# Performance work log

Measured on AMD Instinct MI355X. Metric: run time of the kernel, lower is better.

## Reference

```python
import jax, jax.numpy as jnp
import numpy as np

D = 64       # feature_dim
C = 64       # number of classes
NS = 1024    # support samples (16 shots per class)
NQ = 32768   # query samples
REG = 0.3    # reg_param
KAPPA0 = 1.0 / 600.0  # gamma_m from _num_images=600


def _l2norm(x):
    # torch F.normalize(p=2, dim=1) with eps=1e-12
    return x / jnp.maximum(jnp.linalg.norm(x, axis=1, keepdims=True), 1e-12)


def setup_inputs() -> dict:
    key = jax.random.key(0)
    k1, k2 = jax.random.split(key)
    return {
        "X_support": jax.random.normal(k1, (NS, D), dtype=jnp.float32),
        "y_support": jnp.arange(NS, dtype=jnp.int32) % C,  # every class populated
        "X_query": jax.random.normal(k2, (NQ, D), dtype=jnp.float32),
        "m": jnp.zeros((D,), dtype=jnp.float32),            # zeros * gamma_m
        "S": jnp.eye(D, dtype=jnp.float32),                  # eye * gamma_S
        "nu": jnp.float32(float(D)),
        "kappa": jnp.float32(KAPPA0),
    }


def reference(X_support, y_support, X_query, m, S, nu, kappa):
    # ---- fit ----
    Xs = _l2norm(X_support)                                   # [NS, D]
    onehot = jax.nn.one_hot(y_support, C, dtype=Xs.dtype)     # [NS, C]
    Nj = onehot.sum(axis=0)                                   # [C] per-class counts
    means = (onehot.T @ Xs) / Nj[:, None]                     # [C, D] class means
    N0 = Nj[0]                                                # original uses class-0 count
    # head_mu_eq is vector + scalar broadcast, exactly as the torch code
    head = kappa / (kappa + N0) * m + N0 / (kappa + N0)       # [D]
    mu = head[None, :] * means                                # [C, D] elementwise product
    L = S * jnp.tril(jnp.ones((D, D), dtype=Xs.dtype))        # triu(ones).t() mask
    middle = L @ L.T                                          # [D, D]
    Ssum = jnp.einsum('nj,nd,ne->jde', onehot, Xs, Xs)        # sum of outer products per class
    left = 1.0 / (nu + Nj + D + 2)                            # [C]
    mmT = kappa * jnp.outer(m, m)                             # [D, D]
    mu_outer = jnp.einsum('jd,je->jde', mu, mu)               # [C, D, D]
    right = middle[None] + Ssum + mmT[None] - (kappa + Nj)[:, None, None] * mu_outer
    sigma = left[:, None, None] * right                       # [C, D, D]
    A = (1.0 - REG) * jnp.linalg.inv(sigma) + REG * jnp.eye(D, dtype=Xs.dtype)

    # ---- predict: -(x - mu_j)^T A_j (x - mu_j), A_j symmetric ----
    Xq = _l2norm(X_query)                                     # [NQ, D]
    Amu = jnp.einsum('jde,je->jd', A, mu)                     # [C, D]
    cross = Xq @ Amu.T                                        # [NQ, C]
    muAmu = jnp.einsum('jd,jd->j', mu, Amu)                   # [C]
    XA = jnp.einsum('nd,jde->nje', Xq, A)                     # [NQ, C, D]
    quad = jnp.einsum('nje,ne->nj', XA, Xq)                   # [NQ, C]
    return -(quad - 2.0 * cross + muAmu[None, :])             # [NQ, C]
```

## Files before the change

### kernel.cpp

```cpp
#include <hip/hip_runtime.h>
#include <stdint.h>

#define NSUP 1024
#define NQRY 32768
#define DIM  64
#define NCLS 64

typedef float  f32x4  __attribute__((ext_vector_type(4)));
typedef short  s16x8  __attribute__((ext_vector_type(8)));
typedef __bf16 bf16x8 __attribute__((ext_vector_type(8)));

static __device__ __forceinline__ unsigned short f2bf(float f) {
  unsigned u = __float_as_uint(f);
  u += 0x7FFFu + ((u >> 16) & 1u);
  return (unsigned short)(u >> 16);
}
static __device__ __forceinline__ float rl(float v, int l) {
  return __uint_as_float(__builtin_amdgcn_readlane(__float_as_uint(v), l));
}
static __device__ __forceinline__ float rcp_nr(float x) {
  float r = __builtin_amdgcn_rcpf(x);
  return r * fmaf(-x, r, 2.0f);
}
static __device__ __forceinline__ float rsq_nr(float x) {
  float r = __builtin_amdgcn_rsqf(x);
  return r * fmaf(-0.5f * x * r, r, 1.5f);
}

__global__ __launch_bounds__(256) void prep_and_mid(
    const float* __restrict__ Xq, const float* __restrict__ mg,
    const float* __restrict__ Sg, const float* __restrict__ kapg,
    unsigned short* __restrict__ Ybf, float* __restrict__ Mid2) {
  __shared__ float Sls[64 * 65];
  __shared__ float mls[64];
  int tid = threadIdx.x;

  if (blockIdx.x < 2048) {
    int lane = tid & 63;
    int wave = tid >> 6;
    int row  = blockIdx.x * 16 + wave * 4 + (lane >> 4);
    int cb   = (lane & 15) * 4;
    float4 v = *(const float4*)(Xq + (size_t)row * 64 + cb);
    float ss = v.x * v.x + v.y * v.y + v.z * v.z + v.w * v.w;
    ss += __shfl_xor(ss, 1);
    ss += __shfl_xor(ss, 2);
    ss += __shfl_xor(ss, 4);
    ss += __shfl_xor(ss, 8);
    float inv = rcp_nr(fmaxf(__builtin_amdgcn_sqrtf(ss), 1e-12f));
    unsigned short a = f2bf(v.x * inv), b = f2bf(v.y * inv);
    unsigned short c = f2bf(v.z * inv), d = f2bf(v.w * inv);
    uint2 o;
    o.x = (unsigned)a | ((unsigned)b << 16);
    o.y = (unsigned)c | ((unsigned)d << 16);
    *(uint2*)(Ybf + (size_t)row * 64 + cb) = o;
    return;
  }

  for (int i = tid; i < 4096; i += 256) Sls[(i >> 6) * 65 + (i & 63)] = Sg[i];
  if (tid < 64) mls[tid] = mg[tid];
  __syncthreads();
  float kap = kapg[0];
  int r_ = tid & 63, cblk = tid >> 6, c0 = cblk * 16;
#pragma unroll 1
  for (int i = 0; i < 16; ++i) {
    int cc = c0 + i;
    int kmax = min(r_, cc);
    float mid = 0.f;
    for (int k = 0; k <= kmax; ++k) mid += Sls[r_ * 65 + k] * Sls[cc * 65 + k];
    Mid2[r_ * 64 + cc] = mid + kap * mls[r_] * mls[cc];
  }
}

__global__ __launch_bounds__(64) void fit_classes(
    const float* __restrict__ Xs, const int* __restrict__ ys,
    const float* __restrict__ mg, const float* __restrict__ Mid2,
    const float* __restrict__ nug, const float* __restrict__ kapg,
    unsigned short* __restrict__ LtG, float* __restrict__ Bg) {
  __shared__ int   lst[NSUP];
  __shared__ float Lls[64 * 68];

  int r = threadIdx.x;
  int j = blockIdx.x;

  int cnt = 0, n0 = 0;
  for (int b = 0; b < NSUP; b += 64) {
    int yv = ys[b + r];
    unsigned long long mj = __ballot(yv == j);
    unsigned long long m0 = __ballot(yv == 0);
    n0 += (int)__popcll(m0);
    if (yv == j) {
      int rank = cnt + (int)__popcll(mj & ((1ull << r) - 1ull));
      lst[rank] = b + r;
    }
    cnt += (int)__popcll(mj);
  }
  __syncthreads();

  float a[64];
  {
    const float* mrow = Mid2 + r * 64;
#pragma unroll
    for (int c4 = 0; c4 < 16; ++c4) {
      float4 v = *(const float4*)(mrow + c4 * 4);
      a[c4 * 4 + 0] = v.x; a[c4 * 4 + 1] = v.y;
      a[c4 * 4 + 2] = v.z; a[c4 * 4 + 3] = v.w;
    }
  }

  float sumx = 0.f;
  for (int s = 0; s < cnt; ++s) {
    int n = lst[s];
    float v = Xs[(size_t)n * 64 + r];
    float ss = v * v;
    ss += __shfl_xor(ss, 1);  ss += __shfl_xor(ss, 2);
    ss += __shfl_xor(ss, 4);  ss += __shfl_xor(ss, 8);
    ss += __shfl_xor(ss, 16); ss += __shfl_xor(ss, 32);
    float inv = rcp_nr(fmaxf(__builtin_amdgcn_sqrtf(ss), 1e-12f));
    float xn = v * inv;
    sumx += xn;
#pragma unroll
    for (int c = 0; c < 64; ++c) a[c] = fmaf(xn, rl(xn, c), a[c]);
  }

  float kap = kapg[0], nuv = nug[0];
  float Njf = (float)cnt, N0f = (float)n0;
  float rkn0 = rcp_nr(kap + N0f);
  float head = kap * rkn0 * mg[r] + N0f * rkn0;
  float mu = head * (sumx * rcp_nr(Njf));

  {
    float left = rcp_nr(nuv + Njf + (float)DIM + 2.0f);
    float t = (kap + Njf) * mu;
#pragma unroll
    for (int c = 0; c < 64; ++c)
      a[c] = left * fmaf(-t, rl(mu, c), a[c]);
  }

  float fr = a[0];
  for (int p = 0; p < 64; ++p) {
    float dval = rl(fr, p);
    float dinv = rcp_nr(dval);
    bool isp = (r == p);
    float frd = fr * dinv;
    float colp_v = isp ? dinv : -frd;
    float fnext = 0.f;
#pragma unroll
    for (int c = 0; c < 64; ++c) {
      float pc = rl(a[c], p);
      float q  = pc * dinv;
      float nv;
      if (c == p) {
        nv = colp_v;
      } else {
        float tmp = fmaf(-fr, q, a[c]);
        nv = isp ? q : tmp;
      }
      a[c] = nv;
      if (c == p + 1) fnext = nv;
    }
    fr = fnext;
  }

#pragma unroll
  for (int c = 0; c < 64; ++c) {
    float dd = (c == r) ? 0.3f : 0.f;
    a[c] = fmaf(0.7f, a[c], dd);
  }

  float fk = a[0];
  for (int k = 0; k < 64; ++k) {
    float akk = rl(fk, k);
    float rs  = rsq_nr(akk);
    float lrk = (r >= k) ? fk * rs : 0.f;
    float fnext = 0.f;
#pragma unroll
    for (int c = 0; c < 64; ++c) {
      float nv;
      if (c == k) nv = lrk;
      else        nv = fmaf(-lrk, rl(lrk, c), a[c]);
      a[c] = nv;
      if (c == k + 1) fnext = nv;
    }
    fk = fnext;
  }

#pragma unroll
  for (int c = 0; c < 64; ++c)
    Lls[r * 68 + c] = (c <= r) ? a[c] : 0.f;
  __syncthreads();

  unsigned short* lrow = LtG + (size_t)j * 4096 + r * 64;
  float bias = 0.f;
#pragma unroll
  for (int u = 0; u < 8; ++u) {
    float v0 = Lls[(u * 8 + 0) * 68 + r];
    float v1 = Lls[(u * 8 + 1) * 68 + r];
    float v2 = Lls[(u * 8 + 2) * 68 + r];
    float v3 = Lls[(u * 8 + 3) * 68 + r];
    float v4 = Lls[(u * 8 + 4) * 68 + r];
    float v5 = Lls[(u * 8 + 5) * 68 + r];
    float v6 = Lls[(u * 8 + 6) * 68 + r];
    float v7 = Lls[(u * 8 + 7) * 68 + r];
    bias = fmaf(v0, rl(mu, u * 8 + 0), bias);
    bias = fmaf(v1, rl(mu, u * 8 + 1), bias);
    bias = fmaf(v2, rl(mu, u * 8 + 2), bias);
    bias = fmaf(v3, rl(mu, u * 8 + 3), bias);
    bias = fmaf(v4, rl(mu, u * 8 + 4), bias);
    bias = fmaf(v5, rl(mu, u * 8 + 5), bias);
    bias = fmaf(v6, rl(mu, u * 8 + 6), bias);
    bias = fmaf(v7, rl(mu, u * 8 + 7), bias);
    uint4 w;
    w.x = (unsigned)f2bf(v0) | ((unsigned)f2bf(v1) << 16);
    w.y = (unsigned)f2bf(v2) | ((unsigned)f2bf(v3) << 16);
    w.z = (unsigned)f2bf(v4) | ((unsigned)f2bf(v5) << 16);
    w.w = (unsigned)f2bf(v6) | ((unsigned)f2bf(v7) << 16);
    *(uint4*)(lrow + u * 8) = w;
  }
  Bg[j * 64 + r] = bias;
}

__global__ __launch_bounds__(256) void predict_kernel(
    const unsigned short* __restrict__ Ybf, const unsigned short* __restrict__ Lt,
    const float* __restrict__ Bg, float* __restrict__ out) {
  __shared__ float scl[256 * 17];
  int tid   = threadIdx.x;
  int lane  = tid & 63;
  int wave  = tid >> 6;
  int qt    = blockIdx.x >> 2;
  int cg    = blockIdx.x & 3;
  int cbase = cg * 16;
  int qbase = qt * 256 + wave * 64;
  int c = lane & 15, h = lane >> 4;

  s16x8 bfr[4][2];
#pragma unroll
  for (int nt = 0; nt < 4; ++nt) {
    const unsigned short* yrow = Ybf + (size_t)(qbase + nt * 16 + c) * 64;
#pragma unroll
    for (int ks = 0; ks < 2; ++ks)
      bfr[nt][ks] = *(const s16x8*)(yrow + ks * 32 + h * 8);
  }

  const unsigned short* ab    = Lt + (size_t)cbase * 4096 + c * 64 + h * 8;
  const float*          bbase = Bg + (size_t)cbase * 64 + h * 4;
  float*                sbase = &scl[tid * 17];

#pragma unroll 1
  for (int jj = 0; jj < 16; ++jj) {
    const unsigned short* aj = ab + (size_t)jj * 4096;
    s16x8 af0 = *(const s16x8*)(aj + 0);
    s16x8 af1 = *(const s16x8*)(aj + 1024);
    s16x8 af2 = *(const s16x8*)(aj + 32);
    s16x8 af3 = *(const s16x8*)(aj + 1056);
    s16x8 af4 = *(const s16x8*)(aj + 2080);
    s16x8 af5 = *(const s16x8*)(aj + 3104);
    const float* bb = bbase + (size_t)jj * 64;
    float4 b0 = *(const float4*)(bb);
    float4 b1 = *(const float4*)(bb + 16);
    float4 b2 = *(const float4*)(bb + 32);
    float4 b3 = *(const float4*)(bb + 48);
    f32x4 nb0 = {-b0.x, -b0.y, -b0.z, -b0.w};
    f32x4 nb1 = {-b1.x, -b1.y, -b1.z, -b1.w};
    f32x4 nb2 = {-b2.x, -b2.y, -b2.z, -b2.w};
    f32x4 nb3 = {-b3.x, -b3.y, -b3.z, -b3.w};

    float ssel = 0.f;
#pragma unroll
    for (int nt = 0; nt < 4; ++nt) {
      f32x4 a0 = __builtin_amdgcn_mfma_f32_16x16x32_bf16(
          __builtin_bit_cast(bf16x8, af0), __builtin_bit_cast(bf16x8, bfr[nt][0]), nb0, 0, 0, 0);
      a0 = __builtin_amdgcn_mfma_f32_16x16x32_bf16(
          __builtin_bit_cast(bf16x8, af2), __builtin_bit_cast(bf16x8, bfr[nt][1]), a0, 0, 0, 0);
      f32x4 a1 = __builtin_amdgcn_mfma_f32_16x16x32_bf16(
          __builtin_bit_cast(bf16x8, af1), __builtin_bit_cast(bf16x8, bfr[nt][0]), nb1, 0, 0, 0);
      a1 = __builtin_amdgcn_mfma_f32_16x16x32_bf16(
          __builtin_bit_cast(bf16x8, af3), __builtin_bit_cast(bf16x8, bfr[nt][1]), a1, 0, 0, 0);
      f32x4 a2 = __builtin_amdgcn_mfma_f32_16x16x32_bf16(
          __builtin_bit_cast(bf16x8, af4), __builtin_bit_cast(bf16x8, bfr[nt][1]), nb2, 0, 0, 0);
      f32x4 a3 = __builtin_amdgcn_mfma_f32_16x16x32_bf16(
          __builtin_bit_cast(bf16x8, af5), __builtin_bit_cast(bf16x8, bfr[nt][1]), nb3, 0, 0, 0);
      float s = a0[0] * a0[0] + a0[1] * a0[1] + a0[2] * a0[2] + a0[3] * a0[3];
      s += a1[0] * a1[0] + a1[1] * a1[1] + a1[2] * a1[2] + a1[3] * a1[3];
      s += a2[0] * a2[0] + a2[1] * a2[1] + a2[2] * a2[2] + a2[3] * a2[3];
      s += a3[0] * a3[0] + a3[1] * a3[1] + a3[2] * a3[2] + a3[3] * a3[3];
      s += __shfl_xor(s, 16);
      s += __shfl_xor(s, 32);
      if (nt == h) ssel = s;
    }
    sbase[jj] = -ssel;
  }

  float* orow = out + (size_t)(qbase + lane) * 64 + cbase;
#pragma unroll
  for (int g = 0; g < 4; ++g) {
    f32x4 v = { sbase[g * 4 + 0], sbase[g * 4 + 1],
                sbase[g * 4 + 2], sbase[g * 4 + 3] };
    *(f32x4*)(orow + g * 4) = v;
  }
}

extern "C" void kernel_launch(void* const* d_in, const int* in_sizes, int n_in,
                              void* d_out, int out_size, void* d_ws, size_t ws_size,
                              hipStream_t stream) {
  const float* Xs   = (const float*)d_in[0];
  const int*   ys   = (const int*)d_in[1];
  const float* Xq   = (const float*)d_in[2];
  const float* mg   = (const float*)d_in[3];
  const float* Sg   = (const float*)d_in[4];
  const float* nug  = (const float*)d_in[5];
  const float* kapg = (const float*)d_in[6];
  float* out = (float*)d_out;

  unsigned short* Ybf = (unsigned short*)d_ws;
  unsigned short* LtG = Ybf + (size_t)NQRY * 64;
  float* Bg   = (float*)(LtG + (size_t)NCLS * 4096);
  float* Mid2 = Bg + NCLS * 64;

  prep_and_mid<<<dim3(2049), dim3(256), 0, stream>>>(Xq, mg, Sg, kapg, Ybf, Mid2);
  fit_classes<<<dim3(NCLS), dim3(64), 0, stream>>>(Xs, ys, mg, Mid2, nug, kapg,
                                                   LtG, Bg);
  predict_kernel<<<dim3(512), dim3(256), 0, stream>>>(Ybf, LtG, Bg, out);
}
```

Measured before the change: 318.6 us.

## Simplify in-register Gauss-Jordan and Cholesky loops, prefetch next class operands

```diff
diff --git a/kernel.cpp b/kernel.cpp
--- a/kernel.cpp
+++ b/kernel.cpp
@@ -129,59 +129,45 @@
   float mu = head * (sumx * rcp_nr(Njf));
 
   {
-    float left = rcp_nr(nuv + Njf + (float)DIM + 2.0f);
     float t = (kap + Njf) * mu;
 #pragma unroll
     for (int c = 0; c < 64; ++c)
-      a[c] = left * fmaf(-t, rl(mu, c), a[c]);
-  }
-
-  float fr = a[0];
+      a[c] = fmaf(-t, rl(mu, c), a[c]);
+  }
+
+#pragma unroll
   for (int p = 0; p < 64; ++p) {
-    float dval = rl(fr, p);
+    float dval = rl(a[p], p);
     float dinv = rcp_nr(dval);
     bool isp = (r == p);
-    float frd = fr * dinv;
-    float colp_v = isp ? dinv : -frd;
-    float fnext = 0.f;
+    float frd   = isp ? (1.0f - dinv) : a[p] * dinv;
+    float newap = isp ? dinv : -frd;
 #pragma unroll
     for (int c = 0; c < 64; ++c) {
-      float pc = rl(a[c], p);
-      float q  = pc * dinv;
-      float nv;
-      if (c == p) {
-        nv = colp_v;
-      } else {
-        float tmp = fmaf(-fr, q, a[c]);
-        nv = isp ? q : tmp;
-      }
-      a[c] = nv;
-      if (c == p + 1) fnext = nv;
-    }
-    fr = fnext;
-  }
-
-#pragma unroll
-  for (int c = 0; c < 64; ++c) {
-    float dd = (c == r) ? 0.3f : 0.f;
-    a[c] = fmaf(0.7f, a[c], dd);
-  }
-
-  float fk = a[0];
+      if (c == p) continue;
+      a[c] = fmaf(-frd, rl(a[c], p), a[c]);
+    }
+    a[p] = newap;
+  }
+
+  {
+    float scale = 0.7f * (nuv + Njf + (float)DIM + 2.0f);
+#pragma unroll
+    for (int c = 0; c < 64; ++c) {
+      float dd = (c == r) ? 0.3f : 0.f;
+      a[c] = fmaf(scale, a[c], dd);
+    }
+  }
+
+#pragma unroll
   for (int k = 0; k < 64; ++k) {
-    float akk = rl(fk, k);
+    float akk = rl(a[k], k);
     float rs  = rsq_nr(akk);
-    float lrk = (r >= k) ? fk * rs : 0.f;
-    float fnext = 0.f;
-#pragma unroll
-    for (int c = 0; c < 64; ++c) {
-      float nv;
-      if (c == k) nv = lrk;
-      else        nv = fmaf(-lrk, rl(lrk, c), a[c]);
-      a[c] = nv;
-      if (c == k + 1) fnext = nv;
-    }
-    fk = fnext;
+    float lrk = (r >= k) ? a[k] * rs : 0.f;
+    a[k] = lrk;
+#pragma unroll
+    for (int c = k + 1; c < 64; ++c)
+      a[c] = fmaf(-lrk, rl(lrk, c), a[c]);
   }
 
 #pragma unroll
@@ -245,20 +231,36 @@
   const float*          bbase = Bg + (size_t)cbase * 64 + h * 4;
   float*                sbase = &scl[tid * 17];
 
+  s16x8 af0 = *(const s16x8*)(ab + 0);
+  s16x8 af1 = *(const s16x8*)(ab + 1024);
+  s16x8 af2 = *(const s16x8*)(ab + 32);
+  s16x8 af3 = *(const s16x8*)(ab + 1056);
+  s16x8 af4 = *(const s16x8*)(ab + 2080);
+  s16x8 af5 = *(const s16x8*)(ab + 3104);
+  float4 b0 = *(const float4*)(bbase);
+  float4 b1 = *(const float4*)(bbase + 16);
+  float4 b2 = *(const float4*)(bbase + 32);
+  float4 b3 = *(const float4*)(bbase + 48);
+
 #pragma unroll 1
   for (int jj = 0; jj < 16; ++jj) {
-    const unsigned short* aj = ab + (size_t)jj * 4096;
-    s16x8 af0 = *(const s16x8*)(aj + 0);
-    s16x8 af1 = *(const s16x8*)(aj + 1024);
-    s16x8 af2 = *(const s16x8*)(aj + 32);
-    s16x8 af3 = *(const s16x8*)(aj + 1056);
-    s16x8 af4 = *(const s16x8*)(aj + 2080);
-    s16x8 af5 = *(const s16x8*)(aj + 3104);
-    const float* bb = bbase + (size_t)jj * 64;
-    float4 b0 = *(const float4*)(bb);
-    float4 b1 = *(const float4*)(bb + 16);
-    float4 b2 = *(const float4*)(bb + 32);
-    float4 b3 = *(const float4*)(bb + 48);
+    s16x8 nf0, nf1, nf2, nf3, nf4, nf5;
+    float4 nb0_, nb1_, nb2_, nb3_;
+    if (jj < 15) {
+      const unsigned short* aj = ab + (size_t)(jj + 1) * 4096;
+      nf0 = *(const s16x8*)(aj + 0);
+      nf1 = *(const s16x8*)(aj + 1024);
+      nf2 = *(const s16x8*)(aj + 32);
+      nf3 = *(const s16x8*)(aj + 1056);
+      nf4 = *(const s16x8*)(aj + 2080);
+      nf5 = *(const s16x8*)(aj + 3104);
+      const float* bb = bbase + (size_t)(jj + 1) * 64;
+      nb0_ = *(const float4*)(bb);
+      nb1_ = *(const float4*)(bb + 16);
+      nb2_ = *(const float4*)(bb + 32);
+      nb3_ = *(const float4*)(bb + 48);
+    }
+
     f32x4 nb0 = {-b0.x, -b0.y, -b0.z, -b0.w};
     f32x4 nb1 = {-b1.x, -b1.y, -b1.z, -b1.w};
     f32x4 nb2 = {-b2.x, -b2.y, -b2.z, -b2.w};
@@ -288,6 +290,11 @@
       if (nt == h) ssel = s;
     }
     sbase[jj] = -ssel;
+
+    if (jj < 15) {
+      af0 = nf0; af1 = nf1; af2 = nf2; af3 = nf3; af4 = nf4; af5 = nf5;
+      b0 = nb0_; b1 = nb1_; b2 = nb2_; b3 = nb3_;
+    }
   }
 
   float* orow = out + (size_t)(qbase + lane) * 64 + cbase;
```

Measured after the change: 372.0 us. 16.8% more time.
